# Performance work log

Hardware: AMD Instinct MI355X
Metric: run time of the kernel (lower is better)

## Reference

```python
import jax, jax.numpy as jnp
import numpy as np

VOCAB = 100000
HID = 256
BATCH = 4096
TOTAL_TOKENS = 819200
BN_EPS = 1e-5


def setup_inputs() -> dict:
    key = jax.random.key(0)
    ks = jax.random.split(key, 8)
    token_ids = jax.random.randint(ks[0], (TOTAL_TOKENS,), 0, VOCAB, dtype=jnp.int64)
    segment_ids = jnp.sort(jax.random.randint(ks[1], (TOTAL_TOKENS,), 0, BATCH, dtype=jnp.int64))
    labels = jax.random.uniform(ks[2], (BATCH,), dtype=jnp.float32)
    emb = jax.random.normal(ks[3], (VOCAB, HID), dtype=jnp.float32)
    W1 = jax.random.normal(ks[4], (HID, HID), dtype=jnp.float32) * (1.0 / np.sqrt(HID))
    b1 = jnp.zeros((HID,), dtype=jnp.float32)
    gamma = jnp.ones((HID,), dtype=jnp.float32)
    beta = jnp.zeros((HID,), dtype=jnp.float32)
    W2 = jax.random.normal(ks[5], (1, HID), dtype=jnp.float32) * (1.0 / np.sqrt(HID))
    b2 = jnp.zeros((1,), dtype=jnp.float32)
    return {"token_ids": token_ids, "segment_ids": segment_ids, "labels": labels,
            "emb": emb, "W1": W1, "b1": b1, "gamma": gamma, "beta": beta,
            "W2": W2, "b2": b2}


def reference(token_ids, segment_ids, labels, emb, W1, b1, gamma, beta, W2, b2):
    # Ragged embedding gather + per-document mean (fused EmbeddingBag-mean).
    tok_emb = emb[token_ids]                                   # [T, H]
    seg_sum = jax.ops.segment_sum(tok_emb, segment_ids, num_segments=BATCH)  # [B, H]
    counts = jax.ops.segment_sum(jnp.ones((token_ids.shape[0],), tok_emb.dtype),
                                 segment_ids, num_segments=BATCH)            # [B]
    bow = seg_sum / jnp.maximum(counts, 1.0)[:, None]          # [B, H]
    # Linear -> BatchNorm1d (batch stats, biased var) -> ReLU
    h = bow @ W1.T + b1                                        # [B, H]
    mu = jnp.mean(h, axis=0)
    var = jnp.mean((h - mu) ** 2, axis=0)
    h = (h - mu) * jax.lax.rsqrt(var + BN_EPS) * gamma + beta
    h = jax.nn.relu(h)
    # Dropout in eval mode (identity) for deterministic reference.
    logits = (h @ W2.T + b2)[:, 0]                             # [B]
    # BCEWithLogitsLoss (mean), numerically stable form.
    loss = jnp.mean(jnp.maximum(logits, 0.0) - logits * labels
                    + jnp.log1p(jnp.exp(-jnp.abs(logits))))
    return (loss, logits)
```

## Files before the change

kernel.cpp:

```cpp
#include <hip/hip_runtime.h>
#include <hip/hip_fp16.h>
#include <math.h>

#define VOCAB 100000
#define HID 256
#define BATCH 4096
#define BN_EPS 1e-5f
#define TPB1 512

#define WS_SEGSUM 0
#define WS_COUNTS (BATCH * HID)
#define WS_COLSUM (WS_COUNTS + BATCH)
#define WS_COLSQ  (WS_COLSUM + HID)
#define WS_ZERO_FLOATS (WS_COLSQ + HID)
#define WS_EMB16_OFF_BYTES ((size_t)WS_ZERO_FLOATS * 4)
#define WS_FP16_BYTES_NEEDED (WS_EMB16_OFF_BYTES + (size_t)VOCAB * HID * 2)

__global__ __launch_bounds__(256) void k0_convert_zero(
    const float* __restrict__ emb, __half* __restrict__ emb16,
    float4* __restrict__ zws, int n4, int nz4)
{
    int i = blockIdx.x * 256 + threadIdx.x;
    if (i < nz4) zws[i] = make_float4(0.f, 0.f, 0.f, 0.f);
    if (i >= n4) return;
    float4 v = reinterpret_cast<const float4*>(emb)[i];
    __half2 a = __halves2half2(__float2half_rn(v.x), __float2half_rn(v.y));
    __half2 b = __halves2half2(__float2half_rn(v.z), __float2half_rn(v.w));
    uint2 o;
    o.x = __builtin_bit_cast(unsigned int, a);
    o.y = __builtin_bit_cast(unsigned int, b);
    reinterpret_cast<uint2*>(emb16)[i] = o;
}

__global__ __launch_bounds__(256) void k1_gather_fp16(
    const int* __restrict__ token_ids, const int* __restrict__ segment_ids,
    const __half* __restrict__ emb16, float* __restrict__ seg_sum,
    float* __restrict__ counts, int T)
{
    __shared__ int s_tok[TPB1];
    __shared__ int s_seg[TPB1];
    const int tid = threadIdx.x;
    const int t0  = blockIdx.x * TPB1;
    const int n   = min(TPB1, T - t0);
    if (n <= 0) return;
    for (int i = tid; i < n; i += 256) {
        s_tok[i] = token_ids[t0 + i];
        s_seg[i] = segment_ids[t0 + i];
    }
    __syncthreads();

    const int wave = tid >> 6;
    const int lane = tid & 63;
    const int per  = TPB1 / 4;
    const int start = wave * per;
    const int end   = min(start + per, n);
    if (start >= end) return;

    const uint2* __restrict__ embv = reinterpret_cast<const uint2*>(emb16);
    float4 acc = make_float4(0.f, 0.f, 0.f, 0.f);
    int cur = s_seg[start];
    int runlen = 0;

#define K1_FLUSH() do {                                                        \
        float* p = &seg_sum[(size_t)cur * HID + lane * 4];                     \
        atomicAdd(p + 0, acc.x); atomicAdd(p + 1, acc.y);                      \
        atomicAdd(p + 2, acc.z); atomicAdd(p + 3, acc.w);                      \
        if (lane == 0) atomicAdd(&counts[cur], (float)runlen);                 \
        acc = make_float4(0.f, 0.f, 0.f, 0.f); runlen = 0;                     \
    } while (0)

#define K1_PROC16(ii, u) do {                                                  \
        int seg = s_seg[ii];                  \
        if (seg != cur) { K1_FLUSH(); cur = seg; }                             \
        __half2 h01 = __builtin_bit_cast(__half2, (u).x);                      \
        __half2 h23 = __builtin_bit_cast(__half2, (u).y);                      \
        float2 f01 = __half22float2(h01);                                      \
        float2 f23 = __half22float2(h23);                                      \
        acc.x += f01.x; acc.y += f01.y; acc.z += f23.x; acc.w += f23.y;        \
        runlen++;                                                              \
    } while (0)

    const int m8 = start + ((end - start) & ~7);
    for (int i = start; i < m8; i += 8) {
        uint2 u0 = embv[(size_t)s_tok[i + 0] * 64 + lane];
        uint2 u1 = embv[(size_t)s_tok[i + 1] * 64 + lane];
        uint2 u2 = embv[(size_t)s_tok[i + 2] * 64 + lane];
        uint2 u3 = embv[(size_t)s_tok[i + 3] * 64 + lane];
        uint2 u4 = embv[(size_t)s_tok[i + 4] * 64 + lane];
        uint2 u5 = embv[(size_t)s_tok[i + 5] * 64 + lane];
        uint2 u6 = embv[(size_t)s_tok[i + 6] * 64 + lane];
        uint2 u7 = embv[(size_t)s_tok[i + 7] * 64 + lane];
        K1_PROC16(i + 0, u0); K1_PROC16(i + 1, u1);
        K1_PROC16(i + 2, u2); K1_PROC16(i + 3, u3);
        K1_PROC16(i + 4, u4); K1_PROC16(i + 5, u5);
        K1_PROC16(i + 6, u6); K1_PROC16(i + 7, u7);
    }
    for (int i = m8; i < end; ++i) {
        uint2 u = embv[(size_t)s_tok[i] * 64 + lane];
        K1_PROC16(i, u);
    }
    K1_FLUSH();
#undef K1_PROC16
#undef K1_FLUSH
}

__global__ __launch_bounds__(256) void k1_gather_fp32(
    const int* __restrict__ token_ids, const int* __restrict__ segment_ids,
    const float* __restrict__ emb, float* __restrict__ seg_sum,
    float* __restrict__ counts, int T)
{
    __shared__ int s_tok[TPB1];
    __shared__ int s_seg[TPB1];
    const int tid = threadIdx.x;
    const int t0  = blockIdx.x * TPB1;
    const int n   = min(TPB1, T - t0);
    if (n <= 0) return;
    for (int i = tid; i < n; i += 256) {
        s_tok[i] = token_ids[t0 + i];
        s_seg[i] = segment_ids[t0 + i];
    }
    __syncthreads();

    const int wave = tid >> 6;
    const int lane = tid & 63;
    const int per  = TPB1 / 4;
    const int start = wave * per;
    const int end   = min(start + per, n);
    if (start >= end) return;

    const float4* __restrict__ embv = reinterpret_cast<const float4*>(emb);
    float4 acc = make_float4(0.f, 0.f, 0.f, 0.f);
    int cur = s_seg[start];
    int runlen = 0;

#define K1_FLUSH() do {                                                        \
        float* p = &seg_sum[(size_t)cur * HID + lane * 4];                     \
        atomicAdd(p + 0, acc.x); atomicAdd(p + 1, acc.y);                      \
        atomicAdd(p + 2, acc.z); atomicAdd(p + 3, acc.w);                      \
        if (lane == 0) atomicAdd(&counts[cur], (float)runlen);                 \
        acc = make_float4(0.f, 0.f, 0.f, 0.f); runlen = 0;                     \
    } while (0)

#define K1_PROC(ii, v) do {                                                    \
        int seg = s_seg[ii];                                                   \
        if (seg != cur) { K1_FLUSH(); cur = seg; }                             \
        acc.x += (v).x; acc.y += (v).y; acc.z += (v).z; acc.w += (v).w;        \
        runlen++;                                                              \
    } while (0)

    const int m4 = start + ((end - start) & ~3);
    for (int i = start; i < m4; i += 4) {
        float4 a0 = embv[(size_t)s_tok[i + 0] * 64 + lane];
        float4 a1 = embv[(size_t)s_tok[i + 1] * 64 + lane];
        float4 a2 = embv[(size_t)s_tok[i + 2] * 64 + lane];
        float4 a3 = embv[(size_t)s_tok[i + 3] * 64 + lane];
        K1_PROC(i + 0, a0); K1_PROC(i + 1, a1);
        K1_PROC(i + 2, a2); K1_PROC(i + 3, a3);
    }
    for (int i = m4; i < end; ++i) {
        float4 a = embv[(size_t)s_tok[i] * 64 + lane];
        K1_PROC(i, a);
    }
    K1_FLUSH();
#undef K1_PROC
#undef K1_FLUSH
}

#define KT2 32
__global__ __launch_bounds__(256) void k2_gemm_bn(
    const float* seg_sum, const float* __restrict__ counts,
    const float* __restrict__ W1, const float* __restrict__ b1,
    float* hout, float* __restrict__ colsum, float* __restrict__ colsq,
    float* __restrict__ out)
{
    __shared__ float s_bow[16][HID];
    __shared__ float s_w1t[KT2][HID + 1];
    __shared__ float s_cs[HID];
    __shared__ float s_cq[HID];
    const int tid = threadIdx.x;
    const int b0  = blockIdx.x * 16;

    if (blockIdx.x == 0 && tid == 0) out[0] = 0.f;
    s_cs[tid] = 0.f;
    s_cq[tid] = 0.f;

    const float4* ss4 = reinterpret_cast<const float4*>(seg_sum + (size_t)b0 * HID);
#pragma unroll
    for (int p = 0; p < 4; ++p) {
        int f  = p * 256 + tid;
        int r  = f >> 6, k4 = f & 63;
        float inv = 1.f / fmaxf(counts[b0 + r], 1.f);
        float4 v = ss4[f];
        v.x *= inv; v.y *= inv; v.z *= inv; v.w *= inv;
        *reinterpret_cast<float4*>(&s_bow[r][k4 * 4]) = v;
    }

    const int jr = tid >> 3;
    const int q  = tid & 7;
    const float4* __restrict__ W1v = reinterpret_cast<const float4*>(W1);

    float4 pre[8];
#pragma unroll
    for (int pass = 0; pass < 8; ++pass)
        pre[pass] = W1v[(size_t)(pass * 32 + jr) * 64 + q];

    const int cg = tid & 63;
    const int rg = tid >> 6;

    float acc[4][4];
    {
        float4 bj = reinterpret_cast<const float4*>(b1)[cg];
#pragma unroll
        for (int r = 0; r < 4; ++r) {
            acc[r][0] = bj.x; acc[r][1] = bj.y;
            acc[r][2] = bj.z; acc[r][3] = bj.w;
        }
    }

    for (int kt = 0; kt < HID / KT2; ++kt) {
        __syncthreads();
#pragma unroll
        for (int pass = 0; pass < 8; ++pass) {
            int j = pass * 32 + jr;
            float4 w = pre[pass];
            int kl = q * 4;
            s_w1t[kl + 0][j] = w.x;
            s_w1t[kl + 1][j] = w.y;
            s_w1t[kl + 2][j] = w.z;
            s_w1t[kl + 3][j] = w.w;
        }
        __syncthreads();
        if (kt + 1 < HID / KT2) {
#pragma unroll
            for (int pass = 0; pass < 8; ++pass)
                pre[pass] = W1v[(size_t)(pass * 32 + jr) * 64 + (kt + 1) * 8 + q];
        }
#pragma unroll
        for (int ks = 0; ks < 8; ++ks) {
            const int kg = kt * KT2 + ks * 4;
            const int kl = ks * 4;
            float4 bb0 = *reinterpret_cast<const float4*>(&s_bow[rg * 4 + 0][kg]);
            float4 bb1 = *reinterpret_cast<const float4*>(&s_bow[rg * 4 + 1][kg]);
            float4 bb2 = *reinterpret_cast<const float4*>(&s_bow[rg * 4 + 2][kg]);
            float4 bb3 = *reinterpret_cast<const float4*>(&s_bow[rg * 4 + 3][kg]);
            float4 w0 = *reinterpret_cast<const float4*>(&s_w1t[kl + 0][cg * 4]);
            float4 w1 = *reinterpret_cast<const float4*>(&s_w1t[kl + 1][cg * 4]);
            float4 w2 = *reinterpret_cast<const float4*>(&s_w1t[kl + 2][cg * 4]);
            float4 w3 = *reinterpret_cast<const float4*>(&s_w1t[kl + 3][cg * 4]);
#define K2_ROW(r, bb)                                                          \
            acc[r][0] = fmaf(bb.x, w0.x, fmaf(bb.y, w1.x,                      \
                        fmaf(bb.z, w2.x, fmaf(bb.w, w3.x, acc[r][0]))));       \
            acc[r][1] = fmaf(bb.x, w0.y, fmaf(bb.y, w1.y,                      \
                        fmaf(bb.z, w2.y, fmaf(bb.w, w3.y, acc[r][1]))));       \
            acc[r][2] = fmaf(bb.x, w0.z, fmaf(bb.y, w1.z,                      \
                        fmaf(bb.z, w2.z, fmaf(bb.w, w3.z, acc[r][2]))));       \
            acc[r][3] = fmaf(bb.x, w0.w, fmaf(bb.y, w1.w,                      \
                        fmaf(bb.z, w2.w, fmaf(bb.w, w3.w, acc[r][3]))));
            K2_ROW(0, bb0)
            K2_ROW(1, bb1)
            K2_ROW(2, bb2)
            K2_ROW(3, bb3)
#undef K2_ROW
        }
    }

#pragma unroll
    for (int r = 0; r < 4; ++r) {
        float4 v;
        v.x = acc[r][0]; v.y = acc[r][1]; v.z = acc[r][2]; v.w = acc[r][3];
        *reinterpret_cast<float4*>(
            &hout[(size_t)(b0 + rg * 4 + r) * HID + cg * 4]) = v;
    }
#pragma unroll
    for (int c = 0; c < 4; ++c) {
        float ps  = ((acc[0][c] + acc[1][c]) + (acc[2][c] + acc[3][c]));
        float psq = ((acc[0][c] * acc[0][c] + acc[1][c] * acc[1][c])
                   + (acc[2][c] * acc[2][c] + acc[3][c] * acc[3][c]));
        atomicAdd(&s_cs[cg * 4 + c], ps);
        atomicAdd(&s_cq[cg * 4 + c], psq);
    }
    __syncthreads();
    atomicAdd(&colsum[tid], s_cs[tid]);
    atomicAdd(&colsq[tid], s_cq[tid]);
}

__global__ __launch_bounds__(256) void k5_bn_relu_logits_loss(
    const float* __restrict__ hmat,
    const float* __restrict__ colsum, const float* __restrict__ colsq,
    const float* __restrict__ gamma, const float* __restrict__ beta,
    const float* __restrict__ W2, const float* __restrict__ b2,
    const float* __restrict__ labels, float* __restrict__ out)
{
    __shared__ float s_loss[4];
    const int tid  = threadIdx.x;
    const int w    = tid >> 6;
    const int lane = tid & 63;
    const int b0   = blockIdx.x * 16 + w * 4;

    const int j0 = lane, j1 = lane + 64, j2 = lane + 128, j3 = lane + 192;

#define BN_SS(jj, sc, sh) \
    { float mu = colsum[jj] * (1.f / BATCH); \
      float vr = colsq[jj] * (1.f / BATCH) - mu * mu; \
      sc = gamma[jj] * rsqrtf(vr + BN_EPS); \
      sh = beta[jj] - mu * sc; }
    float sc0, sh0, sc1, sh1, sc2, sh2, sc3, sh3;
    BN_SS(j0, sc0, sh0); BN_SS(j1, sc1, sh1);
    BN_SS(j2, sc2, sh2); BN_SS(j3, sc3, sh3);
#undef BN_SS

    const float w0 = W2[j0], w1 = W2[j1], w2v = W2[j2], w3 = W2[j3];
    const float bias2 = b2[0];

    float bce_acc = 0.f;
#pragma unroll
    for (int rr = 0; rr < 4; ++rr) {
        const int b = b0 + rr;
        const float* hr = hmat + (size_t)b * HID;
        float h0 = hr[j0], h1 = hr[j1], h2 = hr[j2], h3 = hr[j3];
        float s = 0.f;
        s += fmaxf(fmaf(h0, sc0, sh0), 0.f) * w0;
        s += fmaxf(fmaf(h1, sc1, sh1), 0.f) * w1;
        s += fmaxf(fmaf(h2, sc2, sh2), 0.f) * w2v;
        s += fmaxf(fmaf(h3, sc3, sh3), 0.f) * w3;
#pragma unroll
        for (int off = 32; off > 0; off >>= 1)
            s += __shfl_down(s, off, 64);
        if (lane == 0) {
            float z = s + bias2;
            out[1 + b] = z;
            float lb = labels[b];
            bce_acc += fmaxf(z, 0.f) - z * lb + log1pf(expf(-fabsf(z)));
        }
    }
    if (lane == 0) s_loss[w] = bce_acc;
    __syncthreads();
    if (tid == 0) {
        float t = (s_loss[0] + s_loss[1]) + (s_loss[2] + s_loss[3]);
        atomicAdd(&out[0], t * (1.f / BATCH));
    }
}

extern "C" void kernel_launch(void* const* d_in, const int* in_sizes, int n_in,
                              void* d_out, int out_size, void* d_ws, size_t ws_size,
                              hipStream_t stream)
{
    const int*   token_ids   = (const int*)d_in[0];
    const int*   segment_ids = (const int*)d_in[1];
    const float* labels      = (const float*)d_in[2];
    const float* emb         = (const float*)d_in[3];
    const float* W1          = (const float*)d_in[4];
    const float* b1          = (const float*)d_in[5];
    const float* gamma       = (const float*)d_in[6];
    const float* beta        = (const float*)d_in[7];
    const float* W2          = (const float*)d_in[8];
    const float* b2          = (const float*)d_in[9];
    float* out = (float*)d_out;
    float* ws  = (float*)d_ws;

    float* seg_sum = ws + WS_SEGSUM;
    float* counts  = ws + WS_COUNTS;
    float* colsum  = ws + WS_COLSUM;
    float* colsq   = ws + WS_COLSQ;

    const int T = in_sizes[0];
    const int g1 = (T + TPB1 - 1) / TPB1;

    if (ws_size >= WS_FP16_BYTES_NEEDED) {
        __half* emb16 = (__half*)((char*)d_ws + WS_EMB16_OFF_BYTES);
        const int n4  = VOCAB * HID / 4;
        const int nz4 = WS_ZERO_FLOATS / 4;
        k0_convert_zero<<<(n4 + 255) / 256, 256, 0, stream>>>(
            emb, emb16, (float4*)d_ws, n4, nz4);
        k1_gather_fp16<<<g1, 256, 0, stream>>>(token_ids, segment_ids, emb16,
                                               seg_sum, counts, T);
    } else {
        hipMemsetAsync(d_ws, 0, (size_t)WS_ZERO_FLOATS * sizeof(float), stream);
        k1_gather_fp32<<<g1, 256, 0, stream>>>(token_ids, segment_ids, emb,
                                               seg_sum, counts, T);
    }
    k2_gemm_bn<<<BATCH / 16, 256, 0, stream>>>(
        seg_sum, counts, W1, b1, seg_sum, colsum, colsq, out);
    k5_bn_relu_logits_loss<<<BATCH / 16, 256, 0, stream>>>(
        seg_sum, colsum, colsq, gamma, beta, W2, b2, labels, out);
}
```

Before: 279.5 us.

## Shard fp16 gather blocks by token-id residue to localize embedding accesses

Each 512-token range is now handled by 8 blocks, and each block keeps only tokens whose id mod 8 equals its shard. The kept tokens are compacted in shared memory with ballot/popcount before the gather. The apparent aim is to improve cache or channel locality of embedding row reads, or to raise parallelism with more, smaller blocks. In exchange it re-reads the token and segment ids 8 times, adds compaction overhead, and multiplies the segment-flush atomics, since each document's tokens are now split across 8 blocks.

```diff
diff --git a/kernel.cpp b/kernel.cpp
--- a/kernel.cpp
+++ b/kernel.cpp
@@ -7,6 +7,7 @@
 #define BATCH 4096
 #define BN_EPS 1e-5f
 #define TPB1 512
+#define NSHARD 8
 
 #define WS_SEGSUM 0
 #define WS_COUNTS (BATCH * HID)
@@ -39,26 +40,58 @@
 {
     __shared__ int s_tok[TPB1];
     __shared__ int s_seg[TPB1];
-    const int tid = threadIdx.x;
-    const int t0  = blockIdx.x * TPB1;
-    const int n   = min(TPB1, T - t0);
+    __shared__ int s_ctok[TPB1];
+    __shared__ int s_cseg[TPB1];
+    __shared__ int s_wsum[8];
+    const int tid   = threadIdx.x;
+    const int range = blockIdx.x >> 3;
+    const int shard = blockIdx.x & 7;
+    const int t0    = range * TPB1;
+    const int n     = min(TPB1, T - t0);
     if (n <= 0) return;
-    for (int i = tid; i < n; i += 256) {
-        s_tok[i] = token_ids[t0 + i];
-        s_seg[i] = segment_ids[t0 + i];
+    for (int i = tid; i < TPB1; i += 256) {
+        int src = min(t0 + i, T - 1);
+        s_tok[i] = token_ids[src];
+        s_seg[i] = segment_ids[src];
     }
     __syncthreads();
 
     const int wave = tid >> 6;
     const int lane = tid & 63;
-    const int per  = TPB1 / 4;
+
+#pragma unroll
+    for (int c = 0; c < 2; ++c) {
+        int i = c * 256 + tid;
+        bool p = (i < n) && ((s_tok[i] & 7) == shard);
+        unsigned long long b = __ballot(p);
+        if (lane == 0) s_wsum[c * 4 + wave] = __popcll(b);
+    }
+    __syncthreads();
+#pragma unroll
+    for (int c = 0; c < 2; ++c) {
+        int i = c * 256 + tid;
+        bool p = (i < n) && ((s_tok[i] & 7) == shard);
+        unsigned long long b = __ballot(p);
+        int gidx = c * 4 + wave;
+        int base = 0;
+        for (int k = 0; k < 8; ++k) base += (k < gidx) ? s_wsum[k] : 0;
+        int pos = base + __popcll(b & ((1ull << lane) - 1ull));
+        if (p) { s_ctok[pos] = s_tok[i]; s_cseg[pos] = s_seg[i]; }
+    }
+    __syncthreads();
+    int m = 0;
+#pragma unroll
+    for (int k = 0; k < 8; ++k) m += s_wsum[k];
+    if (m == 0) return;
+
+    const int per   = (m + 3) >> 2;
     const int start = wave * per;
-    const int end   = min(start + per, n);
+    const int end   = min(start + per, m);
     if (start >= end) return;
 
     const uint2* __restrict__ embv = reinterpret_cast<const uint2*>(emb16);
     float4 acc = make_float4(0.f, 0.f, 0.f, 0.f);
-    int cur = s_seg[start];
+    int cur = s_cseg[start];
     int runlen = 0;
 
 #define K1_FLUSH() do {                                                        \
@@ -70,7 +103,7 @@
     } while (0)
 
 #define K1_PROC16(ii, u) do {                                                  \
-        int seg = s_seg[ii];                  \
+        int seg = s_cseg[ii];                 \
         if (seg != cur) { K1_FLUSH(); cur = seg; }                             \
         __half2 h01 = __builtin_bit_cast(__half2, (u).x);                      \
         __half2 h23 = __builtin_bit_cast(__half2, (u).y);                      \
@@ -80,23 +113,24 @@
         runlen++;                                                              \
     } while (0)
 
+    int i = start;
     const int m8 = start + ((end - start) & ~7);
-    for (int i = start; i < m8; i += 8) {
-        uint2 u0 = embv[(size_t)s_tok[i + 0] * 64 + lane];
-        uint2 u1 = embv[(size_t)s_tok[i + 1] * 64 + lane];
-        uint2 u2 = embv[(size_t)s_tok[i + 2] * 64 + lane];
-        uint2 u3 = embv[(size_t)s_tok[i + 3] * 64 + lane];
-        uint2 u4 = embv[(size_t)s_tok[i + 4] * 64 + lane];
-        uint2 u5 = embv[(size_t)s_tok[i + 5] * 64 + lane];
-        uint2 u6 = embv[(size_t)s_tok[i + 6] * 64 + lane];
-        uint2 u7 = embv[(size_t)s_tok[i + 7] * 64 + lane];
+    for (; i < m8; i += 8) {
+        uint2 u0 = embv[(size_t)s_ctok[i + 0] * 64 + lane];
+        uint2 u1 = embv[(size_t)s_ctok[i + 1] * 64 + lane];
+        uint2 u2 = embv[(size_t)s_ctok[i + 2] * 64 + lane];
+        uint2 u3 = embv[(size_t)s_ctok[i + 3] * 64 + lane];
+        uint2 u4 = embv[(size_t)s_ctok[i + 4] * 64 + lane];
+        uint2 u5 = embv[(size_t)s_ctok[i + 5] * 64 + lane];
+        uint2 u6 = embv[(size_t)s_ctok[i + 6] * 64 + lane];
+        uint2 u7 = embv[(size_t)s_ctok[i + 7] * 64 + lane];
         K1_PROC16(i + 0, u0); K1_PROC16(i + 1, u1);
         K1_PROC16(i + 2, u2); K1_PROC16(i + 3, u3);
         K1_PROC16(i + 4, u4); K1_PROC16(i + 5, u5);
         K1_PROC16(i + 6, u6); K1_PROC16(i + 7, u7);
     }
-    for (int i = m8; i < end; ++i) {
-        uint2 u = embv[(size_t)s_tok[i] * 64 + lane];
+    for (; i < end; ++i) {
+        uint2 u = embv[(size_t)s_ctok[i] * 64 + lane];
         K1_PROC16(i, u);
     }
     K1_FLUSH();
@@ -364,7 +398,7 @@
     float* colsq   = ws + WS_COLSQ;
 
     const int T = in_sizes[0];
-    const int g1 = (T + TPB1 - 1) / TPB1;
+    const int nrange = (T + TPB1 - 1) / TPB1;
 
     if (ws_size >= WS_FP16_BYTES_NEEDED) {
         __half* emb16 = (__half*)((char*)d_ws + WS_EMB16_OFF_BYTES);
@@ -372,12 +406,12 @@
         const int nz4 = WS_ZERO_FLOATS / 4;
         k0_convert_zero<<<(n4 + 255) / 256, 256, 0, stream>>>(
             emb, emb16, (float4*)d_ws, n4, nz4);
-        k1_gather_fp16<<<g1, 256, 0, stream>>>(token_ids, segment_ids, emb16,
-                                               seg_sum, counts, T);
+        k1_gather_fp16<<<nrange * NSHARD, 256, 0, stream>>>(
+            token_ids, segment_ids, emb16, seg_sum, counts, T);
     } else {
         hipMemsetAsync(d_ws, 0, (size_t)WS_ZERO_FLOATS * sizeof(float), stream);
-        k1_gather_fp32<<<g1, 256, 0, stream>>>(token_ids, segment_ids, emb,
-                                               seg_sum, counts, T);
+        k1_gather_fp32<<<nrange, 256, 0, stream>>>(token_ids, segment_ids, emb,
+                                                   seg_sum, counts, T);
     }
     k2_gemm_bn<<<BATCH / 16, 256, 0, stream>>>(
         seg_sum, counts, W1, b1, seg_sum, colsum, colsq, out);
```

Result: slower. 495.4 us (+77.2%).

## Shard fp16 gather across column slices with eight token lanes per wave

Applied to the files above, without the earlier changes.

The fp16 gather kernel now launches eight blocks per 512-token range, each owning one 64-byte column slice of the embedding row. Within a wave, eight lane groups handle interleaved tokens and each lane covers 8 bytes of the slice. The aim is to raise parallelism and memory-level concurrency. In exchange, token and segment IDs are reloaded eight times, and the interleaved token assignment breaks segment runs into more atomic flushes, raising atomic traffic to seg_sum.

```diff
diff --git a/kernel.cpp b/kernel.cpp
--- a/kernel.cpp
+++ b/kernel.cpp
@@ -7,6 +7,7 @@
 #define BATCH 4096
 #define BN_EPS 1e-5f
 #define TPB1 512
+#define NSHARD 8
 
 #define WS_SEGSUM 0
 #define WS_COUNTS (BATCH * HID)
@@ -32,16 +33,18 @@
     reinterpret_cast<uint2*>(emb16)[i] = o;
 }
 
-__global__ __launch_bounds__(256) void k1_gather_fp16(
+__global__ __launch_bounds__(256) void k1_gather_fp16_cs(
     const int* __restrict__ token_ids, const int* __restrict__ segment_ids,
     const __half* __restrict__ emb16, float* __restrict__ seg_sum,
     float* __restrict__ counts, int T)
 {
     __shared__ int s_tok[TPB1];
     __shared__ int s_seg[TPB1];
-    const int tid = threadIdx.x;
-    const int t0  = blockIdx.x * TPB1;
-    const int n   = min(TPB1, T - t0);
+    const int tid   = threadIdx.x;
+    const int range = blockIdx.x >> 3;
+    const int shard = blockIdx.x & 7;
+    const int t0    = range * TPB1;
+    const int n     = min(TPB1, T - t0);
     if (n <= 0) return;
     for (int i = tid; i < n; i += 256) {
         s_tok[i] = token_ids[t0 + i];
@@ -51,26 +54,30 @@
 
     const int wave = tid >> 6;
     const int lane = tid & 63;
+    const int g    = lane >> 3;
+    const int c    = lane & 7;
+    const int col  = shard * 8 + c;
     const int per  = TPB1 / 4;
     const int start = wave * per;
     const int end   = min(start + per, n);
-    if (start >= end) return;
+    int i = start + g;
+    if (i >= end) return;
 
     const uint2* __restrict__ embv = reinterpret_cast<const uint2*>(emb16);
     float4 acc = make_float4(0.f, 0.f, 0.f, 0.f);
-    int cur = s_seg[start];
+    int cur    = s_seg[i];
     int runlen = 0;
 
 #define K1_FLUSH() do {                                                        \
-        float* p = &seg_sum[(size_t)cur * HID + lane * 4];                     \
+        float* p = &seg_sum[(size_t)cur * HID + col * 4];                      \
         atomicAdd(p + 0, acc.x); atomicAdd(p + 1, acc.y);                      \
         atomicAdd(p + 2, acc.z); atomicAdd(p + 3, acc.w);                      \
-        if (lane == 0) atomicAdd(&counts[cur], (float)runlen);                 \
+        if (shard == 0 && c == 0) atomicAdd(&counts[cur], (float)runlen);      \
         acc = make_float4(0.f, 0.f, 0.f, 0.f); runlen = 0;                     \
     } while (0)
 
-#define K1_PROC16(ii, u) do {                                                  \
-        int seg = s_seg[ii];                  \
+#define K1_PROC(ii, u) do {                                                    \
+        int seg = s_seg[ii];                                                   \
         if (seg != cur) { K1_FLUSH(); cur = seg; }                             \
         __half2 h01 = __builtin_bit_cast(__half2, (u).x);                      \
         __half2 h23 = __builtin_bit_cast(__half2, (u).y);                      \
@@ -80,27 +87,22 @@
         runlen++;                                                              \
     } while (0)
 
-    const int m8 = start + ((end - start) & ~7);
-    for (int i = start; i < m8; i += 8) {
-        uint2 u0 = embv[(size_t)s_tok[i + 0] * 64 + lane];
-        uint2 u1 = embv[(size_t)s_tok[i + 1] * 64 + lane];
-        uint2 u2 = embv[(size_t)s_tok[i + 2] * 64 + lane];
-        uint2 u3 = embv[(size_t)s_tok[i + 3] * 64 + lane];
-        uint2 u4 = embv[(size_t)s_tok[i + 4] * 64 + lane];
-        uint2 u5 = embv[(size_t)s_tok[i + 5] * 64 + lane];
-        uint2 u6 = embv[(size_t)s_tok[i + 6] * 64 + lane];
-        uint2 u7 = embv[(size_t)s_tok[i + 7] * 64 + lane];
-        K1_PROC16(i + 0, u0); K1_PROC16(i + 1, u1);
-        K1_PROC16(i + 2, u2); K1_PROC16(i + 3, u3);
-        K1_PROC16(i + 4, u4); K1_PROC16(i + 5, u5);
-        K1_PROC16(i + 6, u6); K1_PROC16(i + 7, u7);
-    }
-    for (int i = m8; i < end; ++i) {
-        uint2 u = embv[(size_t)s_tok[i] * 64 + lane];
-        K1_PROC16(i, u);
+    for (; i + 24 < end; i += 32) {
+        uint2 u0 = embv[(size_t)s_tok[i +  0] * 64 + col];
+        uint2 u1 = embv[(size_t)s_tok[i +  8] * 64 + col];
+        uint2 u2 = embv[(size_t)s_tok[i + 16] * 64 + col];
+        uint2 u3 = embv[(size_t)s_tok[i + 24] * 64 + col];
+        K1_PROC(i +  0, u0);
+        K1_PROC(i +  8, u1);
+        K1_PROC(i + 16, u2);
+        K1_PROC(i + 24, u3);
+    }
+    for (; i < end; i += 8) {
+        uint2 u = embv[(size_t)s_tok[i] * 64 + col];
+        K1_PROC(i, u);
     }
     K1_FLUSH();
-#undef K1_PROC16
+#undef K1_PROC
 #undef K1_FLUSH
 }
 
@@ -364,7 +366,7 @@
     float* colsq   = ws + WS_COLSQ;
 
     const int T = in_sizes[0];
-    const int g1 = (T + TPB1 - 1) / TPB1;
+    const int nrange = (T + TPB1 - 1) / TPB1;
 
     if (ws_size >= WS_FP16_BYTES_NEEDED) {
         __half* emb16 = (__half*)((char*)d_ws + WS_EMB16_OFF_BYTES);
@@ -372,12 +374,12 @@
         const int nz4 = WS_ZERO_FLOATS / 4;
         k0_convert_zero<<<(n4 + 255) / 256, 256, 0, stream>>>(
             emb, emb16, (float4*)d_ws, n4, nz4);
-        k1_gather_fp16<<<g1, 256, 0, stream>>>(token_ids, segment_ids, emb16,
-                                               seg_sum, counts, T);
+        k1_gather_fp16_cs<<<nrange * NSHARD, 256, 0, stream>>>(
+            token_ids, segment_ids, emb16, seg_sum, counts, T);
     } else {
         hipMemsetAsync(d_ws, 0, (size_t)WS_ZERO_FLOATS * sizeof(float), stream);
-        k1_gather_fp32<<<g1, 256, 0, stream>>>(token_ids, segment_ids, emb,
-                                               seg_sum, counts, T);
+        k1_gather_fp32<<<nrange, 256, 0, stream>>>(token_ids, segment_ids, emb,
+                                                   seg_sum, counts, T);
     }
     k2_gemm_bn<<<BATCH / 16, 256, 0, stream>>>(
         seg_sum, counts, W1, b1, seg_sum, colsum, colsq, out);
```

New measurement: 609.2 us. 2.18x slower.
